# Kernel optimization log

Hardware: AMD Instinct MI355X
Metric: run time of the kernel (lower is better)

## Reference

```python
import jax, jax.numpy as jnp
import numpy as np

# pywt bior2.2 decomposition filters (symmetric mode, single-level dwt)
DEC_LO = np.array([0.0, -0.1767766952966369, 0.3535533905932738,
                   1.0606601717798212, 0.3535533905932738, -0.1767766952966369],
                  dtype=np.float32)
DEC_HI = np.array([0.0, 0.3535533905932738, -0.7071067811865476,
                   0.3535533905932738, 0.0, 0.0], dtype=np.float32)


def setup_inputs() -> dict:
    key = jax.random.key(0)
    x = jax.random.normal(key, (32, 64, 16384), dtype=jnp.float32)
    return {"x": x}


def _dwt1d(x):
    """Single-level DWT matching pywt.dwt(sig, 'bior2.2', mode='symmetric').
    x: [B, C, N] -> (a, d) each [B, C, L] with L = (N + F - 1) // 2.
    pywt computes true convolution with the extended signal and keeps odd
    phases; equivalently: symmetric-pad by F-1, drop first sample, then
    stride-2 correlation with the flipped filters.
    """
    B, C, N = x.shape
    F = DEC_LO.shape[0]  # 6
    ext = jnp.pad(x, ((0, 0), (0, 0), (F - 1, F - 1)), mode='symmetric')
    ext = ext[:, :, 1:]  # odd-phase downsampling offset (pywt convention)
    inp = ext.reshape(B * C, 1, -1)  # [B*C, 1, N+2F-3]
    kern = jnp.stack([jnp.asarray(DEC_LO)[::-1],
                      jnp.asarray(DEC_HI)[::-1]])[:, None, :]  # [2, 1, F]
    y = jax.lax.conv_general_dilated(inp, kern, window_strides=(2,),
                                     padding='VALID')  # [B*C, 2, L]
    y = y.reshape(B, C, 2, -1)
    return y[:, :, 0], y[:, :, 1]


def _interp_linear(x, L):
    """torch F.interpolate(mode='linear', align_corners=False) on last dim."""
    N = x.shape[-1]
    src = (jnp.arange(L, dtype=x.dtype) + 0.5) * (N / L) - 0.5
    src = jnp.clip(src, 0.0, N - 1)
    i0 = jnp.floor(src).astype(jnp.int32)
    i1 = jnp.minimum(i0 + 1, N - 1)
    w = (src - i0).astype(x.dtype)
    return x[..., i0] * (1.0 - w) + x[..., i1] * w


def reference(x):
    a, d = _dwt1d(x)                      # [B, C, L] each
    ds = _interp_linear(x, a.shape[-1])   # [B, C, L]
    return jnp.concatenate([ds, a, d], axis=1)  # [B, 3C, L]
```

## Files before the change

kernel.cpp:

```cpp
#include <hip/hip_runtime.h>


namespace {
constexpr int kN = 16384;
constexpr int kL = 8194;
constexpr int kC = 64;
constexpr int kRows = 32 * kC;

__device__ __forceinline__ int symi(int j) {
    j = (j < 0) ? (-j - 1) : j;
    j = (j >= kN) ? (2 * kN - 1 - j) : j;
    return j;
}

__global__ __launch_bounds__(256) void dwt1d_kernel(const float* __restrict__ x,
                                                    float* __restrict__ out) {
    const int k = blockIdx.x * blockDim.x + threadIdx.x;
    const int row = blockIdx.y;
    if (k >= kL) return;

    const float* __restrict__ xr = x + (size_t)row * kN;

    const float LO1 = -0.1767766952966369f;
    const float LO2 = 0.3535533905932738f;
    const float LO3 = 1.0606601717798212f;
    const float HI1 = 0.3535533905932738f;
    const float HI2 = -0.7071067811865476f;

    float v0, v1, v2, v3, v4;
    if (k >= 2 && k <= (kN / 2 - 1)) {
        const float2* p = (const float2*)(xr + 2 * k - 4);
        float2 a0 = p[0];
        float2 a1 = p[1];
        float2 a2 = p[2];
        v0 = a0.x; v1 = a0.y; v2 = a1.x; v3 = a1.y; v4 = a2.x;
    } else {
        const int t = 2 * k;
        v0 = xr[symi(t - 4)];
        v1 = xr[symi(t - 3)];
        v2 = xr[symi(t - 2)];
        v3 = xr[symi(t - 1)];
        v4 = xr[symi(t)];
    }

    const float a = LO3 * v2 + LO2 * (v1 + v3) + LO1 * (v0 + v4);
    const float d = HI2 * v3 + HI1 * (v2 + v4);

    const float scale = 16384.0f / 8194.0f;
    float src = (k + 0.5f) * scale - 0.5f;
    src = fminf(fmaxf(src, 0.0f), (float)(kN - 1));
    int i0 = (int)floorf(src);
    int i1 = min(i0 + 1, kN - 1);
    float w = src - (float)i0;
    const float ds = xr[i0] * (1.0f - w) + xr[i1] * w;

    const int b = row >> 6;
    const int c = row & (kC - 1);
    const size_t base = ((size_t)(b * 192 + c)) * kL + k;
    out[base] = ds;
    out[base + (size_t)64 * kL] = a;
    out[base + (size_t)128 * kL] = d;
}
}

extern "C" void kernel_launch(void* const* d_in, const int* in_sizes, int n_in,
                              void* d_out, int out_size, void* d_ws, size_t ws_size,
                              hipStream_t stream) {
    const float* x = (const float*)d_in[0];
    float* out = (float*)d_out;
    dim3 grid((kL + 255) / 256, kRows);
    dwt1d_kernel<<<grid, dim3(256), 0, stream>>>(x, out);
}
```

Measured before the change: 336.5 us.

## Stage input tile in shared memory and compute eight outputs per thread

Each block now loads a contiguous input tile with float4 into LDS, including symmetric-boundary samples, and then computes eight outputs per thread from shared memory. This replaces the overlapping, unaligned float2 global loads and the scattered interpolation gathers with one coalesced load per tile. It also shrinks the grid. The cost is a __syncthreads, LDS traffic, and fewer blocks per row, which may reduce latency hiding on a kernel that is already bandwidth-bound.

```diff
diff --git a/kernel.cpp b/kernel.cpp
--- a/kernel.cpp
+++ b/kernel.cpp
@@ -4,8 +4,10 @@
 namespace {
 constexpr int kN = 16384;
 constexpr int kL = 8194;
-constexpr int kC = 64;
-constexpr int kRows = 32 * kC;
+constexpr int kTPB = 256;
+constexpr int kOutPerThread = 8;
+constexpr int kTile = kTPB * kOutPerThread;
+constexpr int kStage = 2 * kTile + 8;
 
 __device__ __forceinline__ int symi(int j) {
     j = (j < 0) ? (-j - 1) : j;
@@ -15,51 +17,70 @@
 
 __global__ __launch_bounds__(256) void dwt1d_kernel(const float* __restrict__ x,
                                                     float* __restrict__ out) {
-    const int k = blockIdx.x * blockDim.x + threadIdx.x;
-    const int row = blockIdx.y;
-    if (k >= kL) return;
+    __shared__ float s[kStage];
+
+    const int tile = blockIdx.x;
+    const int row  = blockIdx.y;
+    const int tid  = threadIdx.x;
+    const int k0   = tile * kTile;
+    const int s0   = 2 * k0 - 8;
+    const int lastk = min(kL - 1, k0 + kTile - 1);
+    const int cnt  = 2 * lastk - s0 + 1;
+    const int nchunk = (cnt + 3) >> 2;
 
     const float* __restrict__ xr = x + (size_t)row * kN;
+
+    for (int cck = tid; cck < nchunk; cck += kTPB) {
+        const int g = s0 + 4 * cck;
+        float4 v;
+        if (g >= 0 && g + 3 < kN) {
+            v = *(const float4*)(xr + g);
+        } else {
+            v.x = xr[symi(g)];
+            v.y = xr[symi(g + 1)];
+            v.z = xr[symi(g + 2)];
+            v.w = xr[symi(g + 3)];
+        }
+        *(float4*)(s + 4 * cck) = v;
+    }
+    __syncthreads();
 
     const float LO1 = -0.1767766952966369f;
     const float LO2 = 0.3535533905932738f;
     const float LO3 = 1.0606601717798212f;
     const float HI1 = 0.3535533905932738f;
     const float HI2 = -0.7071067811865476f;
-
-    float v0, v1, v2, v3, v4;
-    if (k >= 2 && k <= (kN / 2 - 1)) {
-        const float2* p = (const float2*)(xr + 2 * k - 4);
-        float2 a0 = p[0];
-        float2 a1 = p[1];
-        float2 a2 = p[2];
-        v0 = a0.x; v1 = a0.y; v2 = a1.x; v3 = a1.y; v4 = a2.x;
-    } else {
-        const int t = 2 * k;
-        v0 = xr[symi(t - 4)];
-        v1 = xr[symi(t - 3)];
-        v2 = xr[symi(t - 2)];
-        v3 = xr[symi(t - 1)];
-        v4 = xr[symi(t)];
-    }
-
-    const float a = LO3 * v2 + LO2 * (v1 + v3) + LO1 * (v0 + v4);
-    const float d = HI2 * v3 + HI1 * (v2 + v4);
-
     const float scale = 16384.0f / 8194.0f;
-    float src = (k + 0.5f) * scale - 0.5f;
-    src = fminf(fmaxf(src, 0.0f), (float)(kN - 1));
-    int i0 = (int)floorf(src);
-    int i1 = min(i0 + 1, kN - 1);
-    float w = src - (float)i0;
-    const float ds = xr[i0] * (1.0f - w) + xr[i1] * w;
 
     const int b = row >> 6;
-    const int c = row & (kC - 1);
-    const size_t base = ((size_t)(b * 192 + c)) * kL + k;
-    out[base] = ds;
-    out[base + (size_t)64 * kL] = a;
-    out[base + (size_t)128 * kL] = d;
+    const int c = row & 63;
+    float* __restrict__ o0 = out + ((size_t)(b * 192 + c)) * kL;
+    float* __restrict__ o1 = o0 + (size_t)64 * kL;
+    float* __restrict__ o2 = o0 + (size_t)128 * kL;
+
+#pragma unroll
+    for (int j = 0; j < kOutPerThread; ++j) {
+        const int kk = k0 + j * kTPB + tid;
+        if (kk >= kL) continue;
+        const int m = 2 * (kk - k0) + 8;
+
+        const float2 q0 = *(const float2*)(s + m - 4);
+        const float2 q1 = *(const float2*)(s + m - 2);
+        const float v4 = s[m];
+        const float a = LO3 * q1.x + LO2 * (q0.y + q1.y) + LO1 * (q0.x + v4);
+        const float d = HI2 * q1.y + HI1 * (q1.x + v4);
+
+        float src = (kk + 0.5f) * scale - 0.5f;
+        src = fminf(fmaxf(src, 0.0f), (float)(kN - 1));
+        const int i0 = (int)floorf(src);
+        const int i1 = min(i0 + 1, kN - 1);
+        const float w = src - (float)i0;
+        const float ds = s[i0 - s0] * (1.0f - w) + s[i1 - s0] * w;
+
+        o0[kk] = ds;
+        o1[kk] = a;
+        o2[kk] = d;
+    }
 }
 }
 
@@ -68,6 +89,6 @@
                               hipStream_t stream) {
     const float* x = (const float*)d_in[0];
     float* out = (float*)d_out;
-    dim3 grid((kL + 255) / 256, kRows);
-    dwt1d_kernel<<<grid, dim3(256), 0, stream>>>(x, out);
+    dim3 grid((kL + kTile - 1) / kTile, 32 * 64);
+    dwt1d_kernel<<<grid, dim3(kTPB), 0, stream>>>(x, out);
 }
```

Measured after the change: 295.4 us. 12.2% less time.
